# Optimization experiments

Hardware: AMD Instinct MI355X
Metric: run time of the kernel (lower is better)

## Reference

```python
import jax, jax.numpy as jnp
import numpy as np

TEMPERATURE = 0.1
INHIBITION = 1.0
TRACE_TAU = 2.0
TRACE_GAIN = 0.5
EPS = 1e-6


def setup_inputs() -> dict:
    key = jax.random.key(0)
    # d2 >= 0 (comes from ReLU upstream per docstring)
    d2 = jax.random.uniform(key, (64, 4096, 64), dtype=jnp.float32)
    return {"d2": d2}


def reference(d2):
    B, L, K = d2.shape
    decay = jnp.exp(jnp.asarray(-1.0 / TRACE_TAU, dtype=d2.dtype))

    def step(z, d2_t):
        # z: [B, K] leaky winner trace; d2_t: [B, K]
        score = d2_t + TRACE_GAIN * z
        soft_w = jax.nn.softmax(score / TEMPERATURE, axis=-1)
        inhibited = jax.nn.relu(soft_w - INHIBITION * soft_w.mean(axis=-1, keepdims=True))
        w_sur = inhibited / (inhibited.sum(axis=-1, keepdims=True) + EPS)
        idx_t = jnp.argmax(score, axis=-1)               # [B]
        hard = jax.nn.one_hot(idx_t, K, dtype=d2_t.dtype)
        z_new = z * decay + jax.lax.stop_gradient(hard)
        return z_new, (idx_t, w_sur)

    z0 = jnp.zeros((B, K), dtype=d2.dtype)
    d2_time = jnp.swapaxes(d2, 0, 1)                     # [L, B, K]
    _, (idx_l, w_sur_l) = jax.lax.scan(step, z0, d2_time)
    idx = jnp.swapaxes(idx_l, 0, 1)                      # [B, L]
    w_sur = jnp.swapaxes(w_sur_l, 0, 1)                  # [B, L, K]

    hard_w = jax.nn.one_hot(idx, K, dtype=d2.dtype)      # [B, L, K]
    # straight-through: hard forward, soft (w_sur) backward
    w = jax.lax.stop_gradient(hard_w - w_sur) + w_sur
    soma_in = jnp.sum(w * d2, axis=-1)                   # [B, L]
    vals = jnp.sum(hard_w * d2, axis=-1)                 # [B, L]
    return idx, vals, w, soma_in
```

## Files before the change

kernel.cpp:

```cpp
#include <hip/hip_runtime.h>
#include <stdint.h>

#define DECAY   0.6065306597126334f

#define B_DIM 64
#define L_DIM 4096
#define K_DIM 64

template <int CTRL>
__device__ __forceinline__ int dpp_mov(int x) {
    return __builtin_amdgcn_update_dpp(0, x, CTRL, 0xf, 0xf, true);
}

__device__ __forceinline__ float wave_max_to63(float x) {
    x = fmaxf(x, __int_as_float(dpp_mov<0x111>(__float_as_int(x))));
    x = fmaxf(x, __int_as_float(dpp_mov<0x112>(__float_as_int(x))));
    x = fmaxf(x, __int_as_float(dpp_mov<0x114>(__float_as_int(x))));
    x = fmaxf(x, __int_as_float(dpp_mov<0x118>(__float_as_int(x))));
    x = fmaxf(x, __int_as_float(dpp_mov<0x142>(__float_as_int(x))));
    x = fmaxf(x, __int_as_float(dpp_mov<0x143>(__float_as_int(x))));
    return x;
}

__device__ __forceinline__ float rdlane_f(float x, int l) {
    return __int_as_float(__builtin_amdgcn_readlane(__float_as_int(x), l));
}

__global__ __launch_bounds__(64) void k1_seq(const float* __restrict__ d2,
                                             uint2* __restrict__ wmask) {
    const int lane = threadIdx.x;
    const int b    = blockIdx.x;
    const float* p = d2 + ((size_t)b << 18) + lane;

    float buf[16];
#pragma unroll
    for (int u = 0; u < 16; ++u) buf[u] = p[(size_t)u << 6];

    float z = 0.0f;

    for (int g = 0; g < 64; ++g) {
        unsigned wlo = 0u, whi = 0u;
#pragma unroll
        for (int u = 0; u < 64; ++u) {
            const int t = (g << 6) + u;
            float d2v = buf[u & 15];
            int tn = t + 16; if (tn > L_DIM - 1) tn = L_DIM - 1;
            buf[u & 15] = p[(size_t)tn << 6];

            float sc = __builtin_fmaf(0.5f, z, d2v);
            float M  = rdlane_f(wave_max_to63(sc), 63);

            unsigned long long mk = __ballot(sc == M);
            unsigned a = __builtin_amdgcn_mbcnt_lo((unsigned)mk, 0u);
            a = __builtin_amdgcn_mbcnt_hi((unsigned)(mk >> 32), a);
            float h1   = (sc == M) ? 1.0f : 0.0f;
            float hard = (a == 0u) ? h1 : 0.0f;

            z = __fadd_rn(__fmul_rn(z, DECAY), hard);

            unsigned hb = (__float_as_uint(hard) >> 23) & 1u;
            if (u < 32) wlo |= hb << u; else whi |= hb << (u - 32);
        }
        wmask[(((size_t)b << 6) + (size_t)g << 6) + lane] = make_uint2(wlo, whi);
    }
}

__global__ __launch_bounds__(256) void k2_par(const float* __restrict__ d2,
                                              const uint2* __restrict__ wmask,
                                              float* __restrict__ out_idx,
                                              float* __restrict__ out_vals,
                                              float* __restrict__ out_w,
                                              float* __restrict__ out_soma) {
    const int wid   = threadIdx.x >> 6;
    const int lane  = threadIdx.x & 63;
    const int chunk = (blockIdx.x << 2) | wid;
    const int c = chunk & 63;
    const int b = chunk >> 6;
    const size_t row0 = ((size_t)b << 12) + ((size_t)c << 6);

    uint2 wb = wmask[((size_t)chunk << 6) + lane];

    int myw = 0;
#pragma unroll
    for (int s = 0; s < 64; ++s) {
        unsigned bit = (s < 32) ? ((wb.x >> s) & 1u) : ((wb.y >> (s - 32)) & 1u);
        unsigned long long m = __ballot(bit != 0u);
        int w = (int)__ffsll((long long)m) - 1;
        if (lane == s) myw = w;
    }

    out_idx[row0 + lane] = (float)myw;
    float val = d2[((row0 + (size_t)lane) << 6) + myw];
    out_vals[row0 + lane] = val;
    out_soma[row0 + lane] = val;

    float4* pw4 = (float4*)(out_w + (row0 << 6));
    const int sub = lane >> 4;
    const int cb  = (lane & 15) << 2;
#pragma unroll
    for (int j = 0; j < 16; ++j) {
        const int r0 = j << 2;
        int wa = __builtin_amdgcn_readlane(myw, r0 + 0);
        int wbn = __builtin_amdgcn_readlane(myw, r0 + 1);
        int wc = __builtin_amdgcn_readlane(myw, r0 + 2);
        int wd = __builtin_amdgcn_readlane(myw, r0 + 3);
        int t0 = (sub & 2) ? wc : wa;
        int t1 = (sub & 2) ? wd : wbn;
        int wr = (sub & 1) ? t1 : t0;
        float4 v;
        v.x = (cb + 0 == wr) ? 1.0f : 0.0f;
        v.y = (cb + 1 == wr) ? 1.0f : 0.0f;
        v.z = (cb + 2 == wr) ? 1.0f : 0.0f;
        v.w = (cb + 3 == wr) ? 1.0f : 0.0f;
        pw4[(size_t)((r0 + sub) << 4) + (lane & 15)] = v;
    }
}

extern "C" void kernel_launch(void* const* d_in, const int* in_sizes, int n_in,
                              void* d_out, int out_size, void* d_ws, size_t ws_size,
                              hipStream_t stream) {
    (void)in_sizes; (void)n_in; (void)out_size; (void)ws_size;

    const float* d2 = (const float*)d_in[0];
    float* out = (float*)d_out;

    const size_t BL = (size_t)B_DIM * L_DIM;
    float* out_idx  = out;
    float* out_vals = out + BL;
    float* out_w    = out + 2 * BL;
    float* out_soma = out + 2 * BL + BL * K_DIM;

    uint2* wmask = (uint2*)d_ws;

    hipLaunchKernelGGL(k1_seq, dim3(B_DIM), dim3(64), 0, stream, d2, wmask);
    hipLaunchKernelGGL(k2_par, dim3(1024), dim3(256), 0, stream,
                       d2, wmask, out_idx, out_vals, out_w, out_soma);
}
```

Before: 487.1 us.

## Speculate next-step argmax off the serial chain and emit idx/vals from scan kernel

```diff
diff --git a/kernel.cpp b/kernel.cpp
--- a/kernel.cpp
+++ b/kernel.cpp
@@ -22,12 +22,10 @@
     return x;
 }
 
-__device__ __forceinline__ float rdlane_f(float x, int l) {
-    return __int_as_float(__builtin_amdgcn_readlane(__float_as_int(x), l));
-}
-
 __global__ __launch_bounds__(64) void k1_seq(const float* __restrict__ d2,
-                                             uint2* __restrict__ wmask) {
+                                             float* __restrict__ out_idx,
+                                             float* __restrict__ out_vals,
+                                             float* __restrict__ out_soma) {
     const int lane = threadIdx.x;
     const int b    = blockIdx.x;
     const float* p = d2 + ((size_t)b << 18) + lane;
@@ -36,63 +34,68 @@
 #pragma unroll
     for (int u = 0; u < 16; ++u) buf[u] = p[(size_t)u << 6];
 
-    float z = 0.0f;
+    float zd = 0.0f, za = 0.0f;
+    int   w_prev = 63;
+    float spec1 = buf[0];
+    unsigned M0;
+    unsigned long long b0;
+    {
+        float tr = wave_max_to63(buf[0]);
+        M0 = (unsigned)__builtin_amdgcn_readlane(__float_as_int(tr), 63);
+        b0 = __ballot(__float_as_uint(buf[0]) == M0);
+    }
 
-    for (int g = 0; g < 64; ++g) {
-        unsigned wlo = 0u, whi = 0u;
+    int   hold_i = 0;
+    float hold_v = 0.0f;
+
+    for (int g = 0; g < 256; ++g) {
 #pragma unroll
-        for (int u = 0; u < 64; ++u) {
-            const int t = (g << 6) + u;
-            float d2v = buf[u & 15];
+        for (int u = 0; u < 16; ++u) {
+            const int t    = (g << 4) + u;
+            const int slot = ((g & 3) << 4) | u;
+
+            unsigned su = (unsigned)__builtin_amdgcn_readlane(__float_as_int(spec1), w_prev);
+            unsigned long long wbit = 1ull << w_prev;
+            unsigned long long c1   = (su == M0) ? (b0 | wbit) : b0;
+            unsigned long long cand = (su > M0) ? wbit : c1;
+            int w = (int)__ffsll((long long)cand) - 1;
+
+            float z = (lane == w_prev) ? za : zd;
+            zd = __fmul_rn(z, DECAY);
+            za = __fadd_rn(zd, 1.0f);
+            float d2n = buf[(u + 1) & 15];
+            float s0n = __builtin_fmaf(0.5f, zd, d2n);
+            float s1n = __builtin_fmaf(0.5f, za, d2n);
+            float trn = wave_max_to63(s0n);
+            unsigned M0n = (unsigned)__builtin_amdgcn_readlane(__float_as_int(trn), 63);
+            unsigned long long b0n = __ballot(__float_as_uint(s0n) == M0n);
+
+            float d2v = buf[u];
+            unsigned vv = (unsigned)__builtin_amdgcn_readlane(__float_as_int(d2v), w);
+            if (lane == slot) { hold_i = w; hold_v = __uint_as_float(vv); }
+
             int tn = t + 16; if (tn > L_DIM - 1) tn = L_DIM - 1;
-            buf[u & 15] = p[(size_t)tn << 6];
+            buf[u] = p[(size_t)tn << 6];
 
-            float sc = __builtin_fmaf(0.5f, z, d2v);
-            float M  = rdlane_f(wave_max_to63(sc), 63);
-
-            unsigned long long mk = __ballot(sc == M);
-            unsigned a = __builtin_amdgcn_mbcnt_lo((unsigned)mk, 0u);
-            a = __builtin_amdgcn_mbcnt_hi((unsigned)(mk >> 32), a);
-            float h1   = (sc == M) ? 1.0f : 0.0f;
-            float hard = (a == 0u) ? h1 : 0.0f;
-
-            z = __fadd_rn(__fmul_rn(z, DECAY), hard);
-
-            unsigned hb = (__float_as_uint(hard) >> 23) & 1u;
-            if (u < 32) wlo |= hb << u; else whi |= hb << (u - 32);
+            spec1 = s1n; M0 = M0n; b0 = b0n; w_prev = w;
         }
-        wmask[(((size_t)b << 6) + (size_t)g << 6) + lane] = make_uint2(wlo, whi);
+        if ((g & 3) == 3) {
+            size_t o = ((size_t)b << 12) + ((size_t)(g >> 2) << 6) + lane;
+            out_idx[o]  = (float)hold_i;
+            out_vals[o] = hold_v;
+            out_soma[o] = hold_v;
+        }
     }
 }
 
-__global__ __launch_bounds__(256) void k2_par(const float* __restrict__ d2,
-                                              const uint2* __restrict__ wmask,
-                                              float* __restrict__ out_idx,
-                                              float* __restrict__ out_vals,
-                                              float* __restrict__ out_w,
-                                              float* __restrict__ out_soma) {
+__global__ __launch_bounds__(256) void k2_par(const float* __restrict__ in_idx,
+                                              float* __restrict__ out_w) {
     const int wid   = threadIdx.x >> 6;
     const int lane  = threadIdx.x & 63;
     const int chunk = (blockIdx.x << 2) | wid;
-    const int c = chunk & 63;
-    const int b = chunk >> 6;
-    const size_t row0 = ((size_t)b << 12) + ((size_t)c << 6);
+    const size_t row0 = (size_t)chunk << 6;
 
-    uint2 wb = wmask[((size_t)chunk << 6) + lane];
-
-    int myw = 0;
-#pragma unroll
-    for (int s = 0; s < 64; ++s) {
-        unsigned bit = (s < 32) ? ((wb.x >> s) & 1u) : ((wb.y >> (s - 32)) & 1u);
-        unsigned long long m = __ballot(bit != 0u);
-        int w = (int)__ffsll((long long)m) - 1;
-        if (lane == s) myw = w;
-    }
-
-    out_idx[row0 + lane] = (float)myw;
-    float val = d2[((row0 + (size_t)lane) << 6) + myw];
-    out_vals[row0 + lane] = val;
-    out_soma[row0 + lane] = val;
+    int myw = (int)in_idx[row0 + lane];
 
     float4* pw4 = (float4*)(out_w + (row0 << 6));
     const int sub = lane >> 4;
@@ -101,11 +104,11 @@
     for (int j = 0; j < 16; ++j) {
         const int r0 = j << 2;
         int wa = __builtin_amdgcn_readlane(myw, r0 + 0);
-        int wbn = __builtin_amdgcn_readlane(myw, r0 + 1);
+        int wb = __builtin_amdgcn_readlane(myw, r0 + 1);
         int wc = __builtin_amdgcn_readlane(myw, r0 + 2);
         int wd = __builtin_amdgcn_readlane(myw, r0 + 3);
         int t0 = (sub & 2) ? wc : wa;
-        int t1 = (sub & 2) ? wd : wbn;
+        int t1 = (sub & 2) ? wd : wb;
         int wr = (sub & 1) ? t1 : t0;
         float4 v;
         v.x = (cb + 0 == wr) ? 1.0f : 0.0f;
@@ -119,7 +122,7 @@
 extern "C" void kernel_launch(void* const* d_in, const int* in_sizes, int n_in,
                               void* d_out, int out_size, void* d_ws, size_t ws_size,
                               hipStream_t stream) {
-    (void)in_sizes; (void)n_in; (void)out_size; (void)ws_size;
+    (void)in_sizes; (void)n_in; (void)out_size; (void)d_ws; (void)ws_size;
 
     const float* d2 = (const float*)d_in[0];
     float* out = (float*)d_out;
@@ -130,9 +133,8 @@
     float* out_w    = out + 2 * BL;
     float* out_soma = out + 2 * BL + BL * K_DIM;
 
-    uint2* wmask = (uint2*)d_ws;
-
-    hipLaunchKernelGGL(k1_seq, dim3(B_DIM), dim3(64), 0, stream, d2, wmask);
+    hipLaunchKernelGGL(k1_seq, dim3(B_DIM), dim3(64), 0, stream,
+                       d2, out_idx, out_vals, out_soma);
     hipLaunchKernelGGL(k2_par, dim3(1024), dim3(256), 0, stream,
-                       d2, wmask, out_idx, out_vals, out_w, out_soma);
+                       out_idx, out_w);
 }
```

Result: slower. 738.5 us (+51.6%).
